# Kernel optimization log

Measured on AMD Instinct MI355X. Metric: run time of the kernel, lower is better.

Reference implementation:

```python
import jax, jax.numpy as jnp
import numpy as np

CLUSTER_TEMP = 5.0


def setup_inputs() -> dict:
    key = jax.random.key(0)
    ks = jax.random.split(key, 8)
    n, d_in, h, d, K = 50000, 512, 1024, 256, 64
    s = lambda f: 1.0 / np.sqrt(f)
    return {
        "x": jax.random.normal(ks[0], (n, d_in), dtype=jnp.float32),
        "W1": jax.random.normal(ks[1], (d_in, h), dtype=jnp.float32) * s(d_in),
        "b1": jnp.zeros((h,), jnp.float32),
        "W2": jax.random.normal(ks[2], (h, h), dtype=jnp.float32) * s(h),
        "b2": jnp.zeros((h,), jnp.float32),
        "W3": jax.random.normal(ks[3], (h, d), dtype=jnp.float32) * s(h),
        "b3": jnp.zeros((d,), jnp.float32),
        "mu_init": jax.random.normal(ks[4], (K, d), dtype=jnp.float32),
        "num_iter": 10,
    }


def reference(x, W1, b1, W2, b2, W3, b3, mu_init, num_iter):
    # MLP embed: ReLU on all but last layer
    h1 = jax.nn.relu(x @ W1 + b1)
    h2 = jax.nn.relu(h1 @ W2 + b2)
    embeds = h2 @ W3 + b3                      # [n, d]

    # row-wise L2 normalize (torch.diag(1/norm) @ data == row scaling)
    data = embeds / jnp.linalg.norm(embeds, axis=1, keepdims=True)

    def step(mu, _):
        dist = data @ mu.T                     # [n, K]
        r = jax.nn.softmax(CLUSTER_TEMP * dist, axis=1)
        cluster_r = r.sum(axis=0)              # [K]
        cluster_mean = jnp.einsum('nk,nd->kd', r, data)  # [K, d]
        new_mu = cluster_mean / cluster_r[:, None]       # diag(1/cluster_r) @ mean
        return new_mu, None

    mu, _ = jax.lax.scan(step, mu_init, None, length=num_iter)
    dist = data @ mu.T
    r = jax.nn.softmax(CLUSTER_TEMP * dist, axis=1)      # forward returns r only
    return r
```

## Files before the change

kernel.cpp:

```cpp
#include <hip/hip_runtime.h>
#include <math.h>

#define CLUSTER_TEMP 5.0f
#define NSPL 8

typedef __attribute__((ext_vector_type(8))) short bf16x8;
typedef __attribute__((ext_vector_type(4))) float f32x4;

__device__ __forceinline__ unsigned short f2bf(float f) {
  unsigned u = __float_as_uint(f);
  u += 0x7fff + ((u >> 16) & 1);
  return (unsigned short)(u >> 16);
}
__device__ __forceinline__ float bf2f(unsigned short s) {
  return __uint_as_float((unsigned)s << 16);
}

typedef const __attribute__((address_space(1))) void* gas_t;
typedef __attribute__((address_space(3))) void* las_t;
__device__ __forceinline__ void gload16(const void* g, void* l) {
  __builtin_amdgcn_global_load_lds((gas_t)g, (las_t)l, 16, 0, 0);
}

__global__ __launch_bounds__(256)
void wprep(const float* __restrict__ W, unsigned short* __restrict__ hi,
           unsigned short* __restrict__ lo, int K, int N)
{
  __shared__ float tile[32][33];
  const int bx = blockIdx.x * 32;
  const int by = blockIdx.y * 32;
  const int tx = threadIdx.x, ty = threadIdx.y;
#pragma unroll
  for (int i = 0; i < 4; ++i)
    tile[ty + i*8][tx] = W[(size_t)(by + ty + i*8)*N + bx + tx];
  __syncthreads();
#pragma unroll
  for (int i = 0; i < 4; ++i) {
    const int nn = bx + ty + i*8;
    const int kk = by + tx;
    const float v = tile[tx][ty + i*8];
    const unsigned short h = f2bf(v);
    hi[(size_t)nn*K + kk] = h;
    lo[(size_t)nn*K + kk] = f2bf(v - bf2f(h));
  }
}

template<int INMODE, bool RELU, bool PAIR_OUT>
__global__ __launch_bounds__(256, 2)
void gemm_pair(const float* __restrict__ Af,
               const unsigned short* __restrict__ Ah, const unsigned short* __restrict__ Al,
               const unsigned short* __restrict__ Bh, const unsigned short* __restrict__ Bl,
               const float* __restrict__ bias,
               unsigned short* __restrict__ Ch, unsigned short* __restrict__ Cl,
               float* __restrict__ Cf,
               int M, int N, int K)
{
  __shared__ unsigned short As_h[128][32];
  __shared__ unsigned short As_l[128][32];
  __shared__ unsigned short Bs_h[128][32];
  __shared__ unsigned short Bs_l[128][32];
  const int t = threadIdx.x, l = t & 63, w = t >> 6;
  const int wm = w >> 1, wn = w & 1;
  const int fr = l & 15, fq = l >> 4;

  const int gx = gridDim.x;
  const int total = gx * gridDim.y;
  const int flat = blockIdx.y * gx + blockIdx.x;
  const int q = total >> 3, rmd = total & 7;
  const int xcd = flat & 7, pos = flat >> 3;
  const int nid = (xcd < rmd ? xcd * (q + 1) : rmd * (q + 1) + (xcd - rmd) * q) + pos;
  const int row0 = (nid / gx) * 128;
  const int col0 = (nid % gx) * 128;

  const int srow = l >> 2;
  const int scol = (l & 3) * 8;

  f32x4 acc[4][4];
#pragma unroll
  for (int i = 0; i < 4; ++i)
#pragma unroll
    for (int j = 0; j < 4; ++j) {
      acc[i][j][0]=0.f; acc[i][j][1]=0.f; acc[i][j][2]=0.f; acc[i][j][3]=0.f;
    }

  for (int k0 = 0; k0 < K; k0 += 32) {
    __syncthreads();
    if constexpr (INMODE == 0) {
#pragma unroll
      for (int i = 0; i < 4; ++i) {
        const int f = t + i*256;
        const int r = f >> 3, c4 = (f & 7) * 4;
        const int ra = min(row0 + r, M - 1);
        const float4 v = *(const float4*)(Af + (size_t)ra*K + k0 + c4);
        ushort4 hv, lv;
        hv.x = f2bf(v.x); lv.x = f2bf(v.x - bf2f(hv.x));
        hv.y = f2bf(v.y); lv.y = f2bf(v.y - bf2f(hv.y));
        hv.z = f2bf(v.z); lv.z = f2bf(v.z - bf2f(hv.z));
        hv.w = f2bf(v.w); lv.w = f2bf(v.w - bf2f(hv.w));
        *(ushort4*)&As_h[r][c4] = hv;
        *(ushort4*)&As_l[r][c4] = lv;
      }
#pragma unroll
      for (int j = 0; j < 2; ++j) {
        const int chunk = w*2 + j;
        const int rl = chunk*16 + srow;
        const size_t bo = (size_t)(col0 + rl)*K + k0 + scol;
        gload16(Bh + bo, &Bs_h[chunk*16][0]);
        gload16(Bl + bo, &Bs_l[chunk*16][0]);
      }
    } else {
#pragma unroll
      for (int j = 0; j < 2; ++j) {
        const int chunk = w*2 + j;
        const int rl = chunk*16 + srow;
        const int ra = min(row0 + rl, M-1);
        const size_t ao = (size_t)ra*K + k0 + scol;
        const size_t bo = (size_t)(col0 + rl)*K + k0 + scol;
        gload16(Ah + ao, &As_h[chunk*16][0]);
        gload16(Al + ao, &As_l[chunk*16][0]);
        gload16(Bh + bo, &Bs_h[chunk*16][0]);
        gload16(Bl + bo, &Bs_l[chunk*16][0]);
      }
    }
    __syncthreads();

    bf16x8 ah[4], al[4], bh[4], bl[4];
#pragma unroll
    for (int i = 0; i < 4; ++i) {
      ah[i] = *(const bf16x8*)&As_h[wm*64 + i*16 + fr][fq*8];
      al[i] = *(const bf16x8*)&As_l[wm*64 + i*16 + fr][fq*8];
      bh[i] = *(const bf16x8*)&Bs_h[wn*64 + i*16 + fr][fq*8];
      bl[i] = *(const bf16x8*)&Bs_l[wn*64 + i*16 + fr][fq*8];
    }
#pragma unroll
    for (int i = 0; i < 4; ++i)
#pragma unroll
      for (int j = 0; j < 4; ++j) {
        acc[i][j] = __builtin_amdgcn_mfma_f32_16x16x32_bf16(ah[i], bh[j], acc[i][j], 0, 0, 0);
        acc[i][j] = __builtin_amdgcn_mfma_f32_16x16x32_bf16(ah[i], bl[j], acc[i][j], 0, 0, 0);
        acc[i][j] = __builtin_amdgcn_mfma_f32_16x16x32_bf16(al[i], bh[j], acc[i][j], 0, 0, 0);
      }
  }

  float bj[4];
#pragma unroll
  for (int j = 0; j < 4; ++j) bj[j] = bias[col0 + wn*64 + j*16 + fr];

#pragma unroll
  for (int i = 0; i < 4; ++i)
#pragma unroll
    for (int qq = 0; qq < 4; ++qq) {
      const int r = row0 + wm*64 + i*16 + fq*4 + qq;
      if (r < M) {
#pragma unroll
        for (int j = 0; j < 4; ++j) {
          float v = acc[i][j][qq] + bj[j];
          if constexpr (RELU) v = fmaxf(v, 0.f);
          const int cidx = col0 + wn*64 + j*16 + fr;
          if constexpr (PAIR_OUT) {
            const unsigned short h = f2bf(v);
            Ch[(size_t)r*N + cidx] = h;
            Cl[(size_t)r*N + cidx] = f2bf(v - bf2f(h));
          } else {
            Cf[(size_t)r*N + cidx] = v;
          }
        }
      }
    }
}

__global__ __launch_bounds__(256)
void normsplit(const float* __restrict__ E,
               unsigned short* __restrict__ dsph, unsigned short* __restrict__ dspl,
               unsigned short* __restrict__ dshT, unsigned short* __restrict__ dslT,
               int n, int nt)
{
  __shared__ float tile[64][260];
  __shared__ float nrm[4][64];
  __shared__ float invr[64];
  const int t = threadIdx.x;
  const int n0 = blockIdx.x * 64;
#pragma unroll
  for (int i = 0; i < 16; ++i) {
    const int flat = t + i*256;
    const int r = flat >> 6, c4 = (flat & 63) * 4;
    const int rg = min(n0 + r, n - 1);
    *(float4*)&tile[r][c4] = *(const float4*)(E + (size_t)rg*256 + c4);
  }
  __syncthreads();
  {
    const int r = t & 63, qq = t >> 6;
    float s = 0.f;
#pragma unroll
    for (int j = 0; j < 64; ++j) { const float v = tile[r][qq*64 + j]; s = fmaf(v, v, s); }
    nrm[qq][r] = s;
  }
  __syncthreads();
  if (t < 64) invr[t] = 1.0f / sqrtf(nrm[0][t] + nrm[1][t] + nrm[2][t] + nrm[3][t]);
  __syncthreads();
#pragma unroll
  for (int i = 0; i < 16; ++i) {
    const int flat = t + i*256;
    const int r = flat >> 6, c4 = (flat & 63) * 4;
    float4 v = *(const float4*)&tile[r][c4];
    const float iv = invr[r];
    v.x *= iv; v.y *= iv; v.z *= iv; v.w *= iv;
    ushort4 h, lo;
    h.x = f2bf(v.x); lo.x = f2bf(v.x - bf2f(h.x));
    h.y = f2bf(v.y); lo.y = f2bf(v.y - bf2f(h.y));
    h.z = f2bf(v.z); lo.z = f2bf(v.z - bf2f(h.z));
    h.w = f2bf(v.w); lo.w = f2bf(v.w - bf2f(h.w));
    const int rg = n0 + r;
    const int rb = rg >> 4, fr = rg & 15;
    const int ks = c4 >> 5, g = (c4 >> 3) & 3, j = c4 & 7;
    const size_t o = ((size_t)(rb*8 + ks)*64 + g*16 + fr)*8 + j;
    *(ushort4*)(dsph + o) = h;
    *(ushort4*)(dspl + o) = lo;
  }
  const int dd = t >> 3;
  const int nseg = t & 7;
#pragma unroll
  for (int dgrp = 0; dgrp < 8; ++dgrp) {
    const int d = dgrp*32 + dd;
    union { unsigned short s[8]; uint4 u; } hb, lb;
#pragma unroll
    for (int j = 0; j < 8; ++j) {
      const int r = nseg*8 + j;
      const float v = tile[r][d] * invr[r];
      const unsigned short h = f2bf(v);
      hb.s[j] = h; lb.s[j] = f2bf(v - bf2f(h));
    }
    *(uint4*)(dshT + (size_t)d*nt + n0 + nseg*8) = hb.u;
    *(uint4*)(dslT + (size_t)d*nt + n0 + nseg*8) = lb.u;
  }
}

__device__ __forceinline__ size_t mu_off(int k, int d) {
  return ((size_t)((k >> 4)*8 + (d >> 5))*64 + ((d >> 3) & 3)*16 + (k & 15))*8 + (d & 7);
}

__global__ __launch_bounds__(256)
void musplit0(const float* __restrict__ mu0, unsigned short* __restrict__ muPh,
              unsigned short* __restrict__ muPl)
{
  const int i = blockIdx.x*256 + threadIdx.x;
  const int k = i >> 8, d = i & 255;
  const float v = mu0[i];
  const unsigned short h = f2bf(v);
  const size_t o = mu_off(k, d);
  muPh[o] = h; muPl[o] = f2bf(v - bf2f(h));
}

template<bool FINAL>
__global__ __launch_bounds__(256, 2)
void cluster_iter(const unsigned short* __restrict__ dsph, const unsigned short* __restrict__ dspl,
                  const unsigned short* __restrict__ dshT, const unsigned short* __restrict__ dslT,
                  const unsigned short* __restrict__ muPh, const unsigned short* __restrict__ muPl,
                  float* __restrict__ acc_g, float* __restrict__ accr_g,
                  float* __restrict__ out, int n, int nt)
{
  __shared__ unsigned pt[64][132];
  __shared__ float crp[4][64];
  const int t = threadIdx.x, l = t & 63, w = t >> 6;
  const int fr = l & 15, g = l >> 4;
  const int base = blockIdx.x * 128;
  const int rb0 = (base >> 4) + 2*w;

  f32x4 dacc[2][4];
#pragma unroll
  for (int mf = 0; mf < 2; ++mf)
#pragma unroll
    for (int nf = 0; nf < 4; ++nf) {
      dacc[mf][nf][0]=0.f; dacc[mf][nf][1]=0.f; dacc[mf][nf][2]=0.f; dacc[mf][nf][3]=0.f;
    }
#pragma unroll
  for (int ks = 0; ks < 8; ++ks) {
    bf16x8 Ah[2], Al[2];
#pragma unroll
    for (int mf = 0; mf < 2; ++mf) {
      const size_t ao = ((size_t)((rb0 + mf)*8 + ks)*64 + l)*8;
      Ah[mf] = *(const bf16x8*)(dsph + ao);
      Al[mf] = *(const bf16x8*)(dspl + ao);
    }
#pragma unroll
    for (int nf = 0; nf < 4; ++nf) {
      const size_t bo = ((size_t)(nf*8 + ks)*64 + l)*8;
      const bf16x8 Bh = *(const bf16x8*)(muPh + bo);
      const bf16x8 Bl = *(const bf16x8*)(muPl + bo);
#pragma unroll
      for (int mf = 0; mf < 2; ++mf) {
        dacc[mf][nf] = __builtin_amdgcn_mfma_f32_16x16x32_bf16(Ah[mf], Bh, dacc[mf][nf], 0, 0, 0);
        dacc[mf][nf] = __builtin_amdgcn_mfma_f32_16x16x32_bf16(Ah[mf], Bl, dacc[mf][nf], 0, 0, 0);
        dacc[mf][nf] = __builtin_amdgcn_mfma_f32_16x16x32_bf16(Al[mf], Bh, dacc[mf][nf], 0, 0, 0);
      }
    }
  }

  float accr[4] = {0.f, 0.f, 0.f, 0.f};
#pragma unroll
  for (int mf = 0; mf < 2; ++mf) {
    float mx[4], se[4], p[4][4];
#pragma unroll
    for (int r = 0; r < 4; ++r) {
      mx[r] = fmaxf(fmaxf(dacc[mf][0][r], dacc[mf][1][r]),
                    fmaxf(dacc[mf][2][r], dacc[mf][3][r]));
#pragma unroll
      for (int off = 1; off < 16; off <<= 1) mx[r] = fmaxf(mx[r], __shfl_xor(mx[r], off));
      se[r] = 0.f;
    }
#pragma unroll
    for (int nf = 0; nf < 4; ++nf)
#pragma unroll
      for (int r = 0; r < 4; ++r) {
        p[nf][r] = __expf(CLUSTER_TEMP * (dacc[mf][nf][r] - mx[r]));
        se[r] += p[nf][r];
      }
#pragma unroll
    for (int r = 0; r < 4; ++r) {
#pragma unroll
      for (int off = 1; off < 16; off <<= 1) se[r] += __shfl_xor(se[r], off);
      se[r] = 1.0f / se[r];
    }
    if (FINAL) {
#pragma unroll
      for (int r = 0; r < 4; ++r) {
        const int rowg = base + 32*w + mf*16 + 4*g + r;
        if (rowg < n) {
#pragma unroll
          for (int nf = 0; nf < 4; ++nf)
            out[(size_t)rowg*64 + nf*16 + fr] = p[nf][r] * se[r];
        }
      }
    } else {
#pragma unroll
      for (int r = 0; r < 4; ++r) {
        const int rowg = base + 32*w + mf*16 + 4*g + r;
        const float sc = (rowg < n) ? se[r] : 0.f;
#pragma unroll
        for (int nf = 0; nf < 4; ++nf) {
          const float P = p[nf][r] * sc;
          accr[nf] += P;
          const unsigned short h = f2bf(P);
          const unsigned short lo = f2bf(P - bf2f(h));
          pt[nf*16 + fr][32*w + mf*16 + 4*g + r] = ((unsigned)h << 16) | (unsigned)lo;
        }
      }
    }
  }

  if (FINAL) return;

#pragma unroll
  for (int nf = 0; nf < 4; ++nf) {
    accr[nf] += __shfl_xor(accr[nf], 16);
    accr[nf] += __shfl_xor(accr[nf], 32);
  }
  if (l < 16) {
#pragma unroll
    for (int nf = 0; nf < 4; ++nf) crp[w][nf*16 + l] = accr[nf];
  }
  __syncthreads();

  f32x4 acc2[4][4];
#pragma unroll
  for (int i = 0; i < 4; ++i)
#pragma unroll
    for (int j = 0; j < 4; ++j) {
      acc2[i][j][0]=0.f; acc2[i][j][1]=0.f; acc2[i][j][2]=0.f; acc2[i][j][3]=0.f;
    }
#pragma unroll
  for (int ks = 0; ks < 4; ++ks) {
    bf16x8 Ph[4], Pl[4];
#pragma unroll
    for (int mf = 0; mf < 4; ++mf) {
      union { unsigned u[8]; uint4 v[2]; } uu;
      uu.v[0] = *(const uint4*)&pt[mf*16 + fr][ks*32 + 8*g];
      uu.v[1] = *(const uint4*)&pt[mf*16 + fr][ks*32 + 8*g + 4];
      union { unsigned short s[8]; bf16x8 v; } hh, ll;
#pragma unroll
      for (int j = 0; j < 8; ++j) {
        hh.s[j] = (unsigned short)(uu.u[j] >> 16);
        ll.s[j] = (unsigned short)(uu.u[j] & 0xffffu);
      }
      Ph[mf] = hh.v; Pl[mf] = ll.v;
    }
#pragma unroll
    for (int nf = 0; nf < 4; ++nf) {
      const size_t bo = (size_t)(64*w + nf*16 + fr)*nt + base + ks*32 + 8*g;
      const bf16x8 Bh = *(const bf16x8*)(dshT + bo);
      const bf16x8 Bl = *(const bf16x8*)(dslT + bo);
#pragma unroll
      for (int mf = 0; mf < 4; ++mf) {
        acc2[mf][nf] = __builtin_amdgcn_mfma_f32_16x16x32_bf16(Ph[mf], Bh, acc2[mf][nf], 0, 0, 0);
        acc2[mf][nf] = __builtin_amdgcn_mfma_f32_16x16x32_bf16(Ph[mf], Bl, acc2[mf][nf], 0, 0, 0);
        acc2[mf][nf] = __builtin_amdgcn_mfma_f32_16x16x32_bf16(Pl[mf], Bh, acc2[mf][nf], 0, 0, 0);
      }
    }
  }

  float* accs = acc_g + (size_t)(blockIdx.x & (NSPL-1)) * 16448;
#pragma unroll
  for (int mf = 0; mf < 4; ++mf)
#pragma unroll
    for (int nf = 0; nf < 4; ++nf)
#pragma unroll
      for (int r = 0; r < 4; ++r)
        atomicAdd(&accs[(size_t)(mf*16 + 4*g + r)*256 + 64*w + nf*16 + fr],
                  acc2[mf][nf][r]);
  if (t < 64)
    atomicAdd(&accs[16384 + t], crp[0][t] + crp[1][t] + crp[2][t] + crp[3][t]);
}

__global__ __launch_bounds__(256)
void musplit_it(float* __restrict__ acc_g,
                unsigned short* __restrict__ muPh, unsigned short* __restrict__ muPl)
{
  const int k = blockIdx.x;
  const int d = threadIdx.x;
  float v = 0.f, r = 0.f;
#pragma unroll
  for (int c = 0; c < NSPL; ++c) {
    v += acc_g[(size_t)c*16448 + (size_t)k*256 + d];
    r += acc_g[(size_t)c*16448 + 16384 + k];
  }
  v /= r;
  __syncthreads();
  const size_t o = mu_off(k, d);
  const unsigned short h = f2bf(v);
  muPh[o] = h; muPl[o] = f2bf(v - bf2f(h));
#pragma unroll
  for (int c = 0; c < NSPL; ++c)
    acc_g[(size_t)c*16448 + (size_t)k*256 + d] = 0.f;
  if (d < NSPL) acc_g[(size_t)d*16448 + 16384 + k] = 0.f;
}

extern "C" void kernel_launch(void* const* d_in, const int* in_sizes, int n_in,
                              void* d_out, int out_size, void* d_ws, size_t ws_size,
                              hipStream_t stream)
{
  const float* x   = (const float*)d_in[0];
  const float* W1  = (const float*)d_in[1];
  const float* b1  = (const float*)d_in[2];
  const float* W2  = (const float*)d_in[3];
  const float* b2  = (const float*)d_in[4];
  const float* W3  = (const float*)d_in[5];
  const float* b3  = (const float*)d_in[6];
  const float* mu0 = (const float*)d_in[7];
  const int DIN = 512, H = 1024, D = 256, ITERS = 10;
  const int n = in_sizes[0] / DIN;
  const int NP = ((n + 127) / 128) * 128;
  const int NT = (n + 64 + 255) & ~255;
  const int NBK = NP / 128;

  char* ws = (char*)d_ws;
  const size_t MB = 1024*1024;
  const size_t nH2 = (size_t)n * H * 2;
  unsigned short* h1h = (unsigned short*)ws;
  unsigned short* h1l = (unsigned short*)(ws + nH2);
  unsigned short* h2h = (unsigned short*)(ws + 2*nH2);
  unsigned short* h2l = (unsigned short*)(ws + 3*nH2);
  float* data = (float*)ws;
  unsigned short* dsph = (unsigned short*)(ws + 52*MB);
  unsigned short* dspl = (unsigned short*)(ws + 78*MB);
  unsigned short* dshT = (unsigned short*)(ws + 104*MB);
  unsigned short* dslT = (unsigned short*)(ws + 130*MB);
  float* acc_g  = (float*)(ws + 182*MB);
  unsigned short* muPh = (unsigned short*)(ws + 183*MB);
  unsigned short* muPl = (unsigned short*)(ws + 184*MB);

  unsigned short* w1th = (unsigned short*)d_out;
  unsigned short* w1tl = w1th + (size_t)H*DIN;
  unsigned short* w2th = w1tl + (size_t)H*DIN;
  unsigned short* w2tl = w2th + (size_t)H*H;
  unsigned short* w3th = w2tl + (size_t)H*H;
  unsigned short* w3tl = w3th + (size_t)D*H;

  hipMemsetAsync(acc_g, 0, (size_t)NSPL * 16448 * sizeof(float), stream);

  wprep<<<dim3(H/32, DIN/32), dim3(32,8), 0, stream>>>(W1, w1th, w1tl, DIN, H);
  wprep<<<dim3(H/32, H/32),   dim3(32,8), 0, stream>>>(W2, w2th, w2tl, H, H);
  wprep<<<dim3(D/32, H/32),   dim3(32,8), 0, stream>>>(W3, w3th, w3tl, H, D);

  const int gy = (n + 127) / 128;
  gemm_pair<0, true,  true ><<<dim3(H/128, gy), 256, 0, stream>>>(
      x, nullptr, nullptr, w1th, w1tl, b1, h1h, h1l, nullptr, n, H, DIN);
  gemm_pair<1, true,  true ><<<dim3(H/128, gy), 256, 0, stream>>>(
      nullptr, h1h, h1l, w2th, w2tl, b2, h2h, h2l, nullptr, n, H, H);
  gemm_pair<1, false, false><<<dim3(D/128, gy), 256, 0, stream>>>(
      nullptr, h2h, h2l, w3th, w3tl, b3, nullptr, nullptr, data, n, D, H);

  normsplit<<<dim3(NT/64), dim3(256), 0, stream>>>(data, dsph, dspl, dshT, dslT, n, NT);
  musplit0<<<dim3(64), dim3(256), 0, stream>>>(mu0, muPh, muPl);

  for (int it = 0; it < ITERS; ++it) {
    cluster_iter<false><<<dim3(NBK), dim3(256), 0, stream>>>(
        dsph, dspl, dshT, dslT, muPh, muPl, acc_g, nullptr, nullptr, n, NT);
    musplit_it<<<dim3(64), dim3(256), 0, stream>>>(acc_g, muPh, muPl);
  }
  cluster_iter<true><<<dim3(NBK), dim3(256), 0, stream>>>(
      dsph, dspl, dshT, dslT, muPh, muPl, nullptr, nullptr, (float*)d_out, n, NT);
}
```

Baseline: 1.141 ms.

## Add 256x256-tile 512-thread split-bf16 GEMM for layers two and three

Introduces a new gemm8 kernel with 256x256 output tiles, 8 waves, double-buffered direct-to-LDS loads with an explicit vmcnt wait, XCD-aware block remapping, and raised MFMA priority. It replaces gemm_pair for the W2 and W3 layers; the first layer still uses the old kernel. Larger tiles raise arithmetic intensity and cut redundant global reads of the hi/lo operand pairs. In exchange the kernel uses many more accumulator registers (launch bounds 512,2) and larger LDS, and the D=256 layer gets only one column tile, which reduces the number of blocks.

```diff
diff --git a/kernel.cpp b/kernel.cpp
--- a/kernel.cpp
+++ b/kernel.cpp
@@ -151,6 +151,133 @@
 #pragma unroll
     for (int qq = 0; qq < 4; ++qq) {
       const int r = row0 + wm*64 + i*16 + fq*4 + qq;
+      if (r < M) {
+#pragma unroll
+        for (int j = 0; j < 4; ++j) {
+          float v = acc[i][j][qq] + bj[j];
+          if constexpr (RELU) v = fmaxf(v, 0.f);
+          const int cidx = col0 + wn*64 + j*16 + fr;
+          if constexpr (PAIR_OUT) {
+            const unsigned short h = f2bf(v);
+            Ch[(size_t)r*N + cidx] = h;
+            Cl[(size_t)r*N + cidx] = f2bf(v - bf2f(h));
+          } else {
+            Cf[(size_t)r*N + cidx] = v;
+          }
+        }
+      }
+    }
+}
+
+template<bool RELU, bool PAIR_OUT>
+__global__ __launch_bounds__(512, 2)
+void gemm8(const unsigned short* __restrict__ Ah, const unsigned short* __restrict__ Al,
+           const unsigned short* __restrict__ Bh, const unsigned short* __restrict__ Bl,
+           const float* __restrict__ bias,
+           unsigned short* __restrict__ Ch, unsigned short* __restrict__ Cl,
+           float* __restrict__ Cf,
+           int M, int N, int K)
+{
+  __shared__ unsigned short lds[4][2][8192];
+  const int t = threadIdx.x, l = t & 63, w = t >> 6;
+  const int wm = w >> 2, wn = w & 3;
+  const int fr = l & 15, fq = l >> 4;
+  const int fq_eff = ((fq + (fr >> 1)) & 3) * 8;
+
+  const int gx = gridDim.x;
+  const int total = gx * gridDim.y;
+  const int flat = blockIdx.y * gx + blockIdx.x;
+  const int q = total >> 3, rmd = total & 7;
+  const int xcd = flat & 7, pos = flat >> 3;
+  const int nid = (xcd < rmd ? xcd * (q + 1) : rmd * (q + 1) + (xcd - rmd) * q) + pos;
+  const int row0 = (nid / gx) * 256;
+  const int col0 = (nid % gx) * 256;
+
+  const int st_row = w*16 + (l >> 2);
+  const int st_fqs = (((l & 3) - (l >> 3)) & 3) * 8;
+
+  auto STG = [&](int kt, int d) {
+    const int kk = kt*32 + st_fqs;
+#pragma unroll
+    for (int h = 0; h < 2; ++h) {
+      const int ar = min(row0 + h*128 + st_row, M - 1);
+      const int br = col0 + h*128 + st_row;
+      const int lb = h*4096 + w*512;
+      gload16(Ah + (size_t)ar*K + kk, &lds[0][d][lb]);
+      gload16(Al + (size_t)ar*K + kk, &lds[1][d][lb]);
+      gload16(Bh + (size_t)br*K + kk, &lds[2][d][lb]);
+      gload16(Bl + (size_t)br*K + kk, &lds[3][d][lb]);
+    }
+  };
+
+  f32x4 acc[8][4];
+#pragma unroll
+  for (int i = 0; i < 8; ++i)
+#pragma unroll
+    for (int j = 0; j < 4; ++j) {
+      acc[i][j][0]=0.f; acc[i][j][1]=0.f; acc[i][j][2]=0.f; acc[i][j][3]=0.f;
+    }
+
+  const int NKT = K >> 5;
+  STG(0, 0);
+
+  for (int kt = 0; kt < NKT; ++kt) {
+    const int d = kt & 1;
+    if (kt + 1 < NKT) {
+      STG(kt + 1, d ^ 1);
+      __builtin_amdgcn_sched_barrier(0);
+      asm volatile("s_waitcnt vmcnt(8)" ::: "memory");
+    } else {
+      __builtin_amdgcn_sched_barrier(0);
+      asm volatile("s_waitcnt vmcnt(0)" ::: "memory");
+    }
+    __builtin_amdgcn_sched_barrier(0);
+    __builtin_amdgcn_s_barrier();
+    __builtin_amdgcn_sched_barrier(0);
+
+    bf16x8 Bhf[4], Blf[4];
+#pragma unroll
+    for (int j = 0; j < 4; ++j) {
+      const int off = (wn*64 + j*16 + fr)*32 + fq_eff;
+      Bhf[j] = *(const bf16x8*)&lds[2][d][off];
+      Blf[j] = *(const bf16x8*)&lds[3][d][off];
+    }
+#pragma unroll
+    for (int p = 0; p < 4; ++p) {
+      bf16x8 Ahf[2], Alf[2];
+#pragma unroll
+      for (int ii = 0; ii < 2; ++ii) {
+        const int off = (wm*128 + (p*2 + ii)*16 + fr)*32 + fq_eff;
+        Ahf[ii] = *(const bf16x8*)&lds[0][d][off];
+        Alf[ii] = *(const bf16x8*)&lds[1][d][off];
+      }
+      __builtin_amdgcn_s_setprio(1);
+#pragma unroll
+      for (int ii = 0; ii < 2; ++ii) {
+        const int mi = p*2 + ii;
+#pragma unroll
+        for (int j = 0; j < 4; ++j) {
+          acc[mi][j] = __builtin_amdgcn_mfma_f32_16x16x32_bf16(Ahf[ii], Bhf[j], acc[mi][j], 0, 0, 0);
+          acc[mi][j] = __builtin_amdgcn_mfma_f32_16x16x32_bf16(Ahf[ii], Blf[j], acc[mi][j], 0, 0, 0);
+          acc[mi][j] = __builtin_amdgcn_mfma_f32_16x16x32_bf16(Alf[ii], Bhf[j], acc[mi][j], 0, 0, 0);
+        }
+      }
+      __builtin_amdgcn_s_setprio(0);
+    }
+    __builtin_amdgcn_sched_barrier(0);
+    __builtin_amdgcn_s_barrier();
+    __builtin_amdgcn_sched_barrier(0);
+  }
+
+  float bj[4];
+#pragma unroll
+  for (int j = 0; j < 4; ++j) bj[j] = bias[col0 + wn*64 + j*16 + fr];
+
+#pragma unroll
+  for (int i = 0; i < 8; ++i)
+#pragma unroll
+    for (int qq = 0; qq < 4; ++qq) {
+      const int r = row0 + wm*128 + i*16 + fq*4 + qq;
       if (r < M) {
 #pragma unroll
         for (int j = 0; j < 4; ++j) {
@@ -481,13 +608,14 @@
   wprep<<<dim3(H/32, H/32),   dim3(32,8), 0, stream>>>(W2, w2th, w2tl, H, H);
   wprep<<<dim3(D/32, H/32),   dim3(32,8), 0, stream>>>(W3, w3th, w3tl, H, D);
 
-  const int gy = (n + 127) / 128;
-  gemm_pair<0, true,  true ><<<dim3(H/128, gy), 256, 0, stream>>>(
+  const int gy128 = (n + 127) / 128;
+  const int gy256 = (n + 255) / 256;
+  gemm_pair<0, true, true><<<dim3(H/128, gy128), 256, 0, stream>>>(
       x, nullptr, nullptr, w1th, w1tl, b1, h1h, h1l, nullptr, n, H, DIN);
-  gemm_pair<1, true,  true ><<<dim3(H/128, gy), 256, 0, stream>>>(
-      nullptr, h1h, h1l, w2th, w2tl, b2, h2h, h2l, nullptr, n, H, H);
-  gemm_pair<1, false, false><<<dim3(D/128, gy), 256, 0, stream>>>(
-      nullptr, h2h, h2l, w3th, w3tl, b3, nullptr, nullptr, data, n, D, H);
+  gemm8<true,  true ><<<dim3(H/256, gy256), 512, 0, stream>>>(
+      h1h, h1l, w2th, w2tl, b2, h2h, h2l, nullptr, n, H, H);
+  gemm8<false, false><<<dim3(D/256, gy256), 512, 0, stream>>>(
+      h2h, h2l, w3th, w3tl, b3, nullptr, nullptr, data, n, D, H);
 
   normsplit<<<dim3(NT/64), dim3(256), 0, stream>>>(data, dsph, dspl, dshT, dslT, n, NT);
   musplit0<<<dim3(64), dim3(256), 0, stream>>>(mu0, muPh, muPl);
```

Measured after the change: 1.165 ms. 1.02x slower.
